# Performance work log

Measured on AMD Instinct MI355X. Metric: run time of the kernel, lower is better.

Reference implementation:

```python
import jax, jax.numpy as jnp
import numpy as np

V, E, H, T, S = 100000, 256, 512, 48, 2048
HD = H // 2  # per-direction hidden size


def _lstm_dir(x, h0, c0, Wih, Whh, b, reverse):
    # Single-direction LSTM over (S, E) input; PyTorch gate order i,f,g,o.
    def step(carry, xt):
        h, c = carry
        z = xt @ Wih.T + h @ Whh.T + b  # (4*HD,)
        i, f, g, o = jnp.split(z, 4)
        i = jax.nn.sigmoid(i)
        f = jax.nn.sigmoid(f)
        g = jnp.tanh(g)
        o = jax.nn.sigmoid(o)
        c = f * c + i * g
        h = o * jnp.tanh(c)
        return (h, c), h
    _, hs = jax.lax.scan(step, (h0, c0), x, reverse=reverse)
    return hs  # (S, HD)


def setup_inputs() -> dict:
    key = jax.random.key(0)
    ks = jax.random.split(key, 12)
    scale = 1.0 / np.sqrt(HD)
    inp = {
        "sent": jax.random.randint(ks[0], (S,), 0, V),
        "embed_table": jax.random.normal(ks[1], (V, E), jnp.float32),
        "Wih_f": jax.random.normal(ks[2], (4 * HD, E), jnp.float32) * scale,
        "Whh_f": jax.random.normal(ks[3], (4 * HD, HD), jnp.float32) * scale,
        "b_f": jax.random.normal(ks[4], (4 * HD,), jnp.float32) * scale,
        "Wih_b": jax.random.normal(ks[5], (4 * HD, E), jnp.float32) * scale,
        "Whh_b": jax.random.normal(ks[6], (4 * HD, HD), jnp.float32) * scale,
        "b_b": jax.random.normal(ks[7], (4 * HD,), jnp.float32) * scale,
        "W_out": jax.random.normal(ks[8], (T, H), jnp.float32) * (1.0 / np.sqrt(H)),
        "b_out": jnp.zeros((T,), jnp.float32),
        "transitions": jax.random.normal(ks[9], (T, T), jnp.float32) * 0.01,
        "h0": jax.random.normal(ks[10], (2, HD), jnp.float32),
        "c0": jax.random.normal(ks[11], (2, HD), jnp.float32),
    }
    return inp


def reference(sent, embed_table, Wih_f, Whh_f, b_f, Wih_b, Whh_b, b_b,
              W_out, b_out, transitions, h0, c0):
    x = embed_table[sent]  # (S, E)
    hf = _lstm_dir(x, h0[0], c0[0], Wih_f, Whh_f, b_f, False)
    hb = _lstm_dir(x, h0[1], c0[1], Wih_b, Whh_b, b_b, True)
    lstm_out = jnp.concatenate([hf, hb], axis=-1)  # (S, H)
    feats = lstm_out @ W_out.T + b_out  # (S, T) emission scores

    # Viterbi forward pass: scores[i,j] = prev[i] + trans[i,j] + obs[j]
    def vstep(prev, obs):
        scores = prev[:, None] + transitions + obs[None, :]
        return jnp.max(scores, axis=0), jnp.argmax(scores, axis=0)
    prev, bps = jax.lax.scan(vstep, feats[0], feats[1:])  # bps: (S-1, T)

    last = jnp.argmax(prev)

    # Backtrack: reverse scan collects the tag at each timestep in order.
    def back(cur, bp):
        p = bp[cur]
        return p, p
    _, prevs = jax.lax.scan(back, last, bps, reverse=True)  # (S-1,)
    path = jnp.concatenate([prevs, last[None]])  # (S,)
    return path
```

## Files before the change

### kernel.cpp

```cpp
#include <hip/hip_runtime.h>
#include <hip/hip_bf16.h>
#include <math.h>

#define S   2048
#define E   256
#define HD  256
#define NCOL 2048
#define NT  48
#define NWG 16

#define XZ_OFF      ((size_t)0)
#define XZ_BYTES    ((size_t)S * 2048 * 4)
#define LSTM_OFF    (XZ_OFF + XZ_BYTES)
#define LSTM_BYTES  ((size_t)S * 512 * 4)
#define FEATS_OFF   (LSTM_OFF + LSTM_BYTES)
#define FEATS_BYTES ((size_t)S * NT * 4)
#define HCUR2_OFF   (FEATS_OFF + FEATS_BYTES)
#define HCUR2_BYTES ((size_t)2 * 2 * 256 * 8)
#define BPS_OFF     (HCUR2_OFF + HCUR2_BYTES)
#define BPS_BYTES   ((size_t)S * NT)
#define PATHA_OFF   (BPS_OFF + BPS_BYTES)
#define PATHA_BYTES ((size_t)3072 * 32)

__device__ __forceinline__ void st_pair_dev(uint2* p, uint2 v) {
    asm volatile("global_store_dwordx2 %0, %1, off sc0 sc1"
                 :: "v"(p), "v"(v) : "memory");
}

__device__ __forceinline__ bool try_h16(const uint2* p, unsigned want,
                                        float h16[16]) {
    uint4 a, b, c, d, e, f, g, h;
    asm volatile(
        "global_load_dwordx4 %0, %8, off sc0 sc1\n\t"
        "global_load_dwordx4 %1, %8, off offset:16 sc0 sc1\n\t"
        "global_load_dwordx4 %2, %8, off offset:32 sc0 sc1\n\t"
        "global_load_dwordx4 %3, %8, off offset:48 sc0 sc1\n\t"
        "global_load_dwordx4 %4, %8, off offset:64 sc0 sc1\n\t"
        "global_load_dwordx4 %5, %8, off offset:80 sc0 sc1\n\t"
        "global_load_dwordx4 %6, %8, off offset:96 sc0 sc1\n\t"
        "global_load_dwordx4 %7, %8, off offset:112 sc0 sc1\n\t"
        "s_waitcnt vmcnt(0)"
        : "=&v"(a), "=&v"(b), "=&v"(c), "=&v"(d),
          "=&v"(e), "=&v"(f), "=&v"(g), "=&v"(h)
        : "v"(p)
        : "memory");
    const unsigned bad =
        (a.y ^ want) | (a.w ^ want) | (b.y ^ want) | (b.w ^ want) |
        (c.y ^ want) | (c.w ^ want) | (d.y ^ want) | (d.w ^ want) |
        (e.y ^ want) | (e.w ^ want) | (f.y ^ want) | (f.w ^ want) |
        (g.y ^ want) | (g.w ^ want) | (h.y ^ want) | (h.w ^ want);
    if (bad) return false;
    h16[0]  = __uint_as_float(a.x); h16[1]  = __uint_as_float(a.z);
    h16[2]  = __uint_as_float(b.x); h16[3]  = __uint_as_float(b.z);
    h16[4]  = __uint_as_float(c.x); h16[5]  = __uint_as_float(c.z);
    h16[6]  = __uint_as_float(d.x); h16[7]  = __uint_as_float(d.z);
    h16[8]  = __uint_as_float(e.x); h16[9]  = __uint_as_float(e.z);
    h16[10] = __uint_as_float(f.x); h16[11] = __uint_as_float(f.z);
    h16[12] = __uint_as_float(g.x); h16[13] = __uint_as_float(g.z);
    h16[14] = __uint_as_float(h.x); h16[15] = __uint_as_float(h.z);
    return true;
}

__global__ __launch_bounds__(256) void gemm_xz(
    const int* __restrict__ sent, const float* __restrict__ emb,
    const float* __restrict__ Wih_f, const float* __restrict__ Wih_b,
    const float* __restrict__ b_f, const float* __restrict__ b_b,
    float* __restrict__ xz)
{
    __shared__ float As[16][132];
    __shared__ float Bs[16][132];
    const int tid = threadIdx.x;
    const int bm = blockIdx.x * 128;
    const int bn = blockIdx.y * 128;
    const int tx = tid & 15, ty = tid >> 4;
    const int lm = tid >> 1, kq = (tid & 1) * 8;

    const int srow = sent[bm + lm];
    const float* arow = emb + (size_t)srow * E;
    const int bcol = bn + lm;
    const float* brow = (bcol < 1024) ? (Wih_f + (size_t)bcol * E)
                                      : (Wih_b + (size_t)(bcol - 1024) * E);
    float acc[8][8];
#pragma unroll
    for (int i = 0; i < 8; ++i)
#pragma unroll
        for (int j = 0; j < 8; ++j) acc[i][j] = 0.f;

    for (int k0 = 0; k0 < 256; k0 += 16) {
        float4 a0 = *(const float4*)(arow + k0 + kq);
        float4 a1 = *(const float4*)(arow + k0 + kq + 4);
        float4 c0v = *(const float4*)(brow + k0 + kq);
        float4 c1v = *(const float4*)(brow + k0 + kq + 4);
        __syncthreads();
        As[kq + 0][lm] = a0.x; As[kq + 1][lm] = a0.y; As[kq + 2][lm] = a0.z; As[kq + 3][lm] = a0.w;
        As[kq + 4][lm] = a1.x; As[kq + 5][lm] = a1.y; As[kq + 6][lm] = a1.z; As[kq + 7][lm] = a1.w;
        Bs[kq + 0][lm] = c0v.x; Bs[kq + 1][lm] = c0v.y; Bs[kq + 2][lm] = c0v.z; Bs[kq + 3][lm] = c0v.w;
        Bs[kq + 4][lm] = c1v.x; Bs[kq + 5][lm] = c1v.y; Bs[kq + 6][lm] = c1v.z; Bs[kq + 7][lm] = c1v.w;
        __syncthreads();
#pragma unroll
        for (int k = 0; k < 16; ++k) {
            float av[8], bv[8];
            *(float4*)&av[0] = *(const float4*)&As[k][ty * 8];
            *(float4*)&av[4] = *(const float4*)&As[k][ty * 8 + 4];
            *(float4*)&bv[0] = *(const float4*)&Bs[k][tx * 8];
            *(float4*)&bv[4] = *(const float4*)&Bs[k][tx * 8 + 4];
#pragma unroll
            for (int i = 0; i < 8; ++i)
#pragma unroll
                for (int j = 0; j < 8; ++j) acc[i][j] += av[i] * bv[j];
        }
    }
    float bias[8];
    const int cb = bn + tx * 8;
    const float* bptr = (cb < 1024) ? (b_f + cb) : (b_b + cb - 1024);
    *(float4*)&bias[0] = *(const float4*)bptr;
    *(float4*)&bias[4] = *(const float4*)(bptr + 4);
#pragma unroll
    for (int i = 0; i < 8; ++i) {
        const int trow = bm + ty * 8 + i;
        float4 o0, o1;
        o0.x = acc[i][0] + bias[0]; o0.y = acc[i][1] + bias[1];
        o0.z = acc[i][2] + bias[2]; o0.w = acc[i][3] + bias[3];
        o1.x = acc[i][4] + bias[4]; o1.y = acc[i][5] + bias[5];
        o1.z = acc[i][6] + bias[6]; o1.w = acc[i][7] + bias[7];
        *(float4*)(xz + (size_t)trow * NCOL + cb) = o0;
        *(float4*)(xz + (size_t)trow * NCOL + cb + 4) = o1;
    }
}

__global__ void __launch_bounds__(256, 2) lstm_rec(
    const float* __restrict__ Whh_f, const float* __restrict__ Whh_b,
    const float* __restrict__ h0, const float* __restrict__ c0,
    const float* __restrict__ xz, uint2* __restrict__ hcur2,
    float* __restrict__ lstm_out)
{
    __shared__ float red[4][16][8];
    __shared__ float actb[128];
    const int wg = blockIdx.x;
    const int dir = wg >> 3;
    const int wi = wg & 7;
    const int ub = wi * 32;
    const int tid = threadIdx.x;
    const int kg = tid >> 4;
    const int rg = tid & 15;
    const int k0 = kg * 16;
    const float* Whh = dir ? Whh_b : Whh_f;

    float w[8][16];
#pragma unroll
    for (int q = 0; q < 8; ++q) {
        const int lr = rg * 8 + q;
        const int grow = (lr >> 5) * 256 + ub + (lr & 31);
        const float* wr = Whh + (size_t)grow * 256 + k0;
#pragma unroll
        for (int kk = 0; kk < 16; kk += 4) {
            float4 v = *(const float4*)(wr + kk);
            w[q][kk] = v.x; w[q][kk + 1] = v.y; w[q][kk + 2] = v.z; w[q][kk + 3] = v.w;
        }
    }
#pragma unroll
    for (int q = 0; q < 8; ++q)
#pragma unroll
        for (int kk = 0; kk < 16; ++kk)
            asm volatile("" : "+v"(w[q][kk]));

    float cst = 0.f;
    if (tid < 32) {
        cst = c0[dir * 256 + ub + tid];
        uint2 iv;
        iv.x = __float_as_uint(h0[dir * 256 + ub + tid]);
        iv.y = 0u;
        st_pair_dev(hcur2 + (size_t)dir * 256 + ub + tid, iv);
    }
    const int zcol = dir * 1024 + (tid >> 5) * 256 + ub + (tid & 31);

    for (int step = 0; step < S; ++step) {
        float xzv = 0.f;
        if (tid < 128) {
            const int tz = dir ? (S - 1 - step) : step;
            xzv = xz[(size_t)tz * NCOL + zcol];
        }
        const uint2* hb = hcur2 + ((size_t)(step & 1) * 2 + dir) * 256 + k0;
        float h16[16];
        while (!try_h16(hb, (unsigned)step, h16)) {}

        float acc[8];
#pragma unroll
        for (int q = 0; q < 8; ++q) acc[q] = 0.f;
#pragma unroll
        for (int kk = 0; kk < 16; ++kk)
#pragma unroll
            for (int q = 0; q < 8; ++q) acc[q] += w[q][kk] * h16[kk];
#pragma unroll
        for (int q = 0; q < 8; ++q) {
            acc[q] += __shfl_xor(acc[q], 16);
            acc[q] += __shfl_xor(acc[q], 32);
        }
        if ((kg & 3) == 0) {
            const int wv = kg >> 2;
#pragma unroll
            for (int q = 0; q < 8; ++q) red[wv][rg][q] = acc[q];
        }
        __syncthreads();
        if (tid < 128) {
            const int rg2 = tid >> 3, q2 = tid & 7;
            const float z = ((red[0][rg2][q2] + red[1][rg2][q2]) +
                             (red[2][rg2][q2] + red[3][rg2][q2])) + xzv;
            const int gate = tid >> 5;
            actb[tid] = (gate == 2) ? tanhf(z) : (1.f / (1.f + expf(-z)));
        }
        __syncthreads();
        if (tid < 32) {
            const int u = tid;
            const float ig = actb[u];
            const float fg = actb[32 + u];
            const float gg = actb[64 + u];
            const float og = actb[96 + u];
            cst = fg * cst + ig * gg;
            const float h = og * tanhf(cst);
            const int tz = dir ? (S - 1 - step) : step;
            uint2 pv;
            pv.x = __float_as_uint(h);
            pv.y = (unsigned)(step + 1);
            st_pair_dev(hcur2 + ((size_t)((step + 1) & 1) * 2 + dir) * 256 + ub + u, pv);
            lstm_out[(size_t)tz * 512 + dir * 256 + ub + u] = h;
        }
    }
}

__global__ __launch_bounds__(256) void feats_k(
    const float* __restrict__ lstm, const float* __restrict__ Wout,
    const float* __restrict__ bout, float* __restrict__ feats)
{
    const int gid = blockIdx.x * 256 + threadIdx.x;
    if (gid >= S * NT) return;
    const int t = gid / NT, tag = gid - t * NT;
    const float* hr = lstm + (size_t)t * 512;
    const float* wr = Wout + (size_t)tag * 512;
    float s0 = 0, s1 = 0, s2 = 0, s3 = 0;
#pragma unroll 4
    for (int k = 0; k < 512; k += 4) {
        float4 h4 = *(const float4*)(hr + k);
        float4 w4 = *(const float4*)(wr + k);
        s0 += h4.x * w4.x; s1 += h4.y * w4.y;
        s2 += h4.z * w4.z; s3 += h4.w * w4.w;
    }
    feats[gid] = (s0 + s1) + (s2 + s3) + bout[tag];
}

__global__ void __launch_bounds__(256, 1) viterbi_k(
    const float* __restrict__ feats, const float* __restrict__ trans,
    unsigned char* __restrict__ bps, unsigned char* __restrict__ pathA,
    int* __restrict__ out)
{
    __shared__ unsigned char cmap[64][NT];
    __shared__ int SB[65];
    __shared__ int last_s;
    const int tid = threadIdx.x;

    if (tid < 64) {
        const bool actj = tid < NT;
        const int j = actj ? tid : 0;
        float T[NT];
#pragma unroll
        for (int i = 0; i < NT; ++i) T[i] = trans[i * NT + j];
        float vself = feats[j];

        auto STEP = [&](int t, float obs) {
            float b0 = -1e30f, b1 = -1e30f, b2 = -1e30f, b3 = -1e30f;
            int i0 = 0, i1 = 12, i2 = 24, i3 = 36;
#pragma unroll
            for (int r = 0; r < 12; ++r) {
                const float v0 = __shfl(vself, r);
                const float v1 = __shfl(vself, 12 + r);
                const float v2 = __shfl(vself, 24 + r);
                const float v3 = __shfl(vself, 36 + r);
                const float s0 = (v0 + T[r])      + obs;
                const float s1 = (v1 + T[12 + r]) + obs;
                const float s2 = (v2 + T[24 + r]) + obs;
                const float s3 = (v3 + T[36 + r]) + obs;
                if (s0 > b0) { b0 = s0; i0 = r; }
                if (s1 > b1) { b1 = s1; i1 = 12 + r; }
                if (s2 > b2) { b2 = s2; i2 = 24 + r; }
                if (s3 > b3) { b3 = s3; i3 = 36 + r; }
            }
            float best = b0; int bi = i0;
            if (b1 > best) { best = b1; bi = i1; }
            if (b2 > best) { best = b2; bi = i2; }
            if (b3 > best) { best = b3; bi = i3; }
            if (actj) {
                bps[(size_t)(t - 1) * NT + j] = (unsigned char)bi;
                vself = best;
            }
        };

        float o0 = feats[(size_t)1 * NT + j];
        float o1 = feats[(size_t)2 * NT + j];
        float o2 = feats[(size_t)3 * NT + j];
        float o3 = feats[(size_t)4 * NT + j];

        for (int tb = 1; tb < S; tb += 4) {
            const int p0 = (tb + 4 < S) ? (tb + 4) : (S - 1);
            const int p1 = (tb + 5 < S) ? (tb + 5) : (S - 1);
            const int p2 = (tb + 6 < S) ? (tb + 6) : (S - 1);
            const int p3 = (tb + 7 < S) ? (tb + 7) : (S - 1);
            const float n0 = feats[(size_t)p0 * NT + j];
            const float n1 = feats[(size_t)p1 * NT + j];
            const float n2 = feats[(size_t)p2 * NT + j];
            const float n3 = feats[(size_t)p3 * NT + j];

            STEP(tb + 0, o0);
            if (tb + 1 < S) STEP(tb + 1, o1);
            if (tb + 2 < S) STEP(tb + 2, o2);
            if (tb + 3 < S) STEP(tb + 3, o3);

            o0 = n0; o1 = n1; o2 = n2; o3 = n3;
        }
        {
            float b = __shfl(vself, 0); int bi = 0;
#pragma unroll
            for (int q = 1; q < NT; ++q) {
                const float vq = __shfl(vself, q);
                if (vq > b) { b = vq; bi = q; }
            }
            if (tid == 0) last_s = bi;
        }
    }
    __syncthreads();

    int cArr[12], sArr[12];
    unsigned char stv[12];
#pragma unroll
    for (int r = 0; r < 12; ++r) {
        const int task = r * 256 + tid;
        cArr[r] = task / NT;
        sArr[r] = task - cArr[r] * NT;
        stv[r] = (unsigned char)sArr[r];
    }
    for (int stp = 31; stp >= 0; --stp) {
#pragma unroll
        for (int r = 0; r < 12; ++r) {
            const int km = cArr[r] * 32 + stp;
            if (km < S - 1) stv[r] = bps[(size_t)km * NT + stv[r]];
            pathA[(size_t)(cArr[r] * NT + sArr[r]) * 32 + stp] = stv[r];
        }
    }
#pragma unroll
    for (int r = 0; r < 12; ++r) cmap[cArr[r]][sArr[r]] = stv[r];
    __syncthreads();
    if (tid == 0) {
        SB[64] = last_s;
        for (int c = 63; c >= 0; --c) SB[c] = cmap[c][SB[c + 1]];
    }
    __syncthreads();
    for (int t = tid; t < S; t += 256) {
        const int c = t >> 5;
        out[t] = (int)pathA[(size_t)(c * NT + SB[c + 1]) * 32 + (t & 31)];
    }
}

extern "C" void kernel_launch(void* const* d_in, const int* in_sizes, int n_in,
                              void* d_out, int out_size, void* d_ws, size_t ws_size,
                              hipStream_t stream) {
    const int*   sent   = (const int*)d_in[0];
    const float* emb    = (const float*)d_in[1];
    const float* Wih_f  = (const float*)d_in[2];
    const float* Whh_f  = (const float*)d_in[3];
    const float* b_f    = (const float*)d_in[4];
    const float* Wih_b  = (const float*)d_in[5];
    const float* Whh_b  = (const float*)d_in[6];
    const float* b_b    = (const float*)d_in[7];
    const float* W_out  = (const float*)d_in[8];
    const float* b_out  = (const float*)d_in[9];
    const float* trans  = (const float*)d_in[10];
    const float* h0     = (const float*)d_in[11];
    const float* c0     = (const float*)d_in[12];
    int* out = (int*)d_out;

    char* ws = (char*)d_ws;
    float* xz       = (float*)(ws + XZ_OFF);
    float* lstm     = (float*)(ws + LSTM_OFF);
    float* feats    = (float*)(ws + FEATS_OFF);
    uint2* hcur2    = (uint2*)(ws + HCUR2_OFF);
    unsigned char* bps   = (unsigned char*)(ws + BPS_OFF);
    unsigned char* pathA = (unsigned char*)(ws + PATHA_OFF);

    hipMemsetAsync(hcur2, 0xFF, HCUR2_BYTES, stream);

    gemm_xz<<<dim3(16, 16), 256, 0, stream>>>(sent, emb, Wih_f, Wih_b, b_f, b_b, xz);

    lstm_rec<<<dim3(NWG), 256, 0, stream>>>(Whh_f, Whh_b, h0, c0, xz, hcur2, lstm);

    feats_k<<<dim3((S * NT + 255) / 256), 256, 0, stream>>>(lstm, W_out, b_out, feats);

    viterbi_k<<<dim3(1), 256, 0, stream>>>(feats, trans, bps, pathA, out);
}
```

Before: 5.437 ms.

## Remove LDS reductions and barriers from LSTM recurrence via wave-local shuffle reduction

Each wave now owns whole hidden units: lanes split only along the K dimension and are reduced with xor shuffles. Every lane then holds the full gate pre-activations for two units and computes the cell update itself. This removes both per-step __syncthreads and the shared-memory staging. The trade-off is that every lane redundantly loads eight xz values and computes activations, and launch bounds drop to one workgroup per CU.

```diff
diff --git a/kernel.cpp b/kernel.cpp
--- a/kernel.cpp
+++ b/kernel.cpp
@@ -128,29 +128,30 @@
     }
 }
 
-__global__ void __launch_bounds__(256, 2) lstm_rec(
+__global__ void __launch_bounds__(256, 1) lstm_rec(
     const float* __restrict__ Whh_f, const float* __restrict__ Whh_b,
     const float* __restrict__ h0, const float* __restrict__ c0,
     const float* __restrict__ xz, uint2* __restrict__ hcur2,
     float* __restrict__ lstm_out)
 {
-    __shared__ float red[4][16][8];
-    __shared__ float actb[128];
-    const int wg = blockIdx.x;
-    const int dir = wg >> 3;
-    const int wi = wg & 7;
-    const int ub = wi * 32;
-    const int tid = threadIdx.x;
-    const int kg = tid >> 4;
-    const int rg = tid & 15;
-    const int k0 = kg * 16;
+    const int wg   = blockIdx.x;
+    const int dir  = wg >> 3;
+    const int wi   = wg & 7;
+    const int tid  = threadIdx.x;
+    const int wave = tid >> 6;
+    const int lane = tid & 63;
+    const int kg   = lane >> 2;
+    const int rql  = lane & 3;
+    const int k0   = kg * 16;
+    const int ubase = wi * 32 + wave * 8;
+    const int u0 = ubase + rql * 2;
+    const int u1 = u0 + 1;
     const float* Whh = dir ? Whh_b : Whh_f;
 
     float w[8][16];
 #pragma unroll
     for (int q = 0; q < 8; ++q) {
-        const int lr = rg * 8 + q;
-        const int grow = (lr >> 5) * 256 + ub + (lr & 31);
+        const int grow = (q & 3) * 256 + u0 + (q >> 2);
         const float* wr = Whh + (size_t)grow * 256 + k0;
 #pragma unroll
         for (int kk = 0; kk < 16; kk += 4) {
@@ -164,22 +165,29 @@
         for (int kk = 0; kk < 16; ++kk)
             asm volatile("" : "+v"(w[q][kk]));
 
-    float cst = 0.f;
-    if (tid < 32) {
-        cst = c0[dir * 256 + ub + tid];
+    float cst0 = c0[dir * 256 + u0];
+    float cst1 = c0[dir * 256 + u1];
+
+    if (kg == 0) {
         uint2 iv;
-        iv.x = __float_as_uint(h0[dir * 256 + ub + tid]);
-        iv.y = 0u;
-        st_pair_dev(hcur2 + (size_t)dir * 256 + ub + tid, iv);
-    }
-    const int zcol = dir * 1024 + (tid >> 5) * 256 + ub + (tid & 31);
+        iv.x = __float_as_uint(h0[dir * 256 + u0]); iv.y = 0u;
+        st_pair_dev(hcur2 + (size_t)dir * 256 + u0, iv);
+        iv.x = __float_as_uint(h0[dir * 256 + u1]); iv.y = 0u;
+        st_pair_dev(hcur2 + (size_t)dir * 256 + u1, iv);
+    }
+
+    int zc[8];
+#pragma unroll
+    for (int q = 0; q < 8; ++q)
+        zc[q] = dir * 1024 + (q & 3) * 256 + u0 + (q >> 2);
 
     for (int step = 0; step < S; ++step) {
-        float xzv = 0.f;
-        if (tid < 128) {
-            const int tz = dir ? (S - 1 - step) : step;
-            xzv = xz[(size_t)tz * NCOL + zcol];
-        }
+        const int tz = dir ? (S - 1 - step) : step;
+        float xzv[8];
+        const float* xrow = xz + (size_t)tz * NCOL;
+#pragma unroll
+        for (int q = 0; q < 8; ++q) xzv[q] = xrow[zc[q]];
+
         const uint2* hb = hcur2 + ((size_t)(step & 1) * 2 + dir) * 256 + k0;
         float h16[16];
         while (!try_h16(hb, (unsigned)step, h16)) {}
@@ -193,37 +201,43 @@
             for (int q = 0; q < 8; ++q) acc[q] += w[q][kk] * h16[kk];
 #pragma unroll
         for (int q = 0; q < 8; ++q) {
+            acc[q] += __shfl_xor(acc[q], 4);
+            acc[q] += __shfl_xor(acc[q], 8);
             acc[q] += __shfl_xor(acc[q], 16);
             acc[q] += __shfl_xor(acc[q], 32);
         }
-        if ((kg & 3) == 0) {
-            const int wv = kg >> 2;
-#pragma unroll
-            for (int q = 0; q < 8; ++q) red[wv][rg][q] = acc[q];
-        }
-        __syncthreads();
-        if (tid < 128) {
-            const int rg2 = tid >> 3, q2 = tid & 7;
-            const float z = ((red[0][rg2][q2] + red[1][rg2][q2]) +
-                             (red[2][rg2][q2] + red[3][rg2][q2])) + xzv;
-            const int gate = tid >> 5;
-            actb[tid] = (gate == 2) ? tanhf(z) : (1.f / (1.f + expf(-z)));
-        }
-        __syncthreads();
-        if (tid < 32) {
-            const int u = tid;
-            const float ig = actb[u];
-            const float fg = actb[32 + u];
-            const float gg = actb[64 + u];
-            const float og = actb[96 + u];
-            cst = fg * cst + ig * gg;
-            const float h = og * tanhf(cst);
-            const int tz = dir ? (S - 1 - step) : step;
+        const float zi0 = acc[0] + xzv[0];
+        const float zf0 = acc[1] + xzv[1];
+        const float zg0 = acc[2] + xzv[2];
+        const float zo0 = acc[3] + xzv[3];
+        const float zi1 = acc[4] + xzv[4];
+        const float zf1 = acc[5] + xzv[5];
+        const float zg1 = acc[6] + xzv[6];
+        const float zo1 = acc[7] + xzv[7];
+        const float ig0 = 1.f / (1.f + expf(-zi0));
+        const float fg0 = 1.f / (1.f + expf(-zf0));
+        const float gg0 = tanhf(zg0);
+        const float og0 = 1.f / (1.f + expf(-zo0));
+        const float ig1 = 1.f / (1.f + expf(-zi1));
+        const float fg1 = 1.f / (1.f + expf(-zf1));
+        const float gg1 = tanhf(zg1);
+        const float og1 = 1.f / (1.f + expf(-zo1));
+        cst0 = fg0 * cst0 + ig0 * gg0;
+        cst1 = fg1 * cst1 + ig1 * gg1;
+        const float hv0 = og0 * tanhf(cst0);
+        const float hv1 = og1 * tanhf(cst1);
+
+        if (kg == 0) {
+            const unsigned tg = (unsigned)(step + 1);
+            uint2* dst = hcur2 + ((size_t)((step + 1) & 1) * 2 + dir) * 256;
             uint2 pv;
-            pv.x = __float_as_uint(h);
-            pv.y = (unsigned)(step + 1);
-            st_pair_dev(hcur2 + ((size_t)((step + 1) & 1) * 2 + dir) * 256 + ub + u, pv);
-            lstm_out[(size_t)tz * 512 + dir * 256 + ub + u] = h;
+            pv.x = __float_as_uint(hv0); pv.y = tg;
+            st_pair_dev(dst + u0, pv);
+            pv.x = __float_as_uint(hv1); pv.y = tg;
+            st_pair_dev(dst + u1, pv);
+            float* lp = lstm_out + (size_t)tz * 512 + dir * 256;
+            lp[u0] = hv0;
+            lp[u1] = hv1;
         }
     }
 }
```

New measurement: 9.458 ms. 1.74x slower.
